# Performance work log

Measured on AMD Instinct MI355X. Metric: run time of the kernel, lower is better.

The kernel has to match this reference:

```python
import jax, jax.numpy as jnp
import numpy as np

B, N, D = 8, 2048, 512   # batch, ctx_size, input_size
P, H = 16, 32            # num_pers, hidden_size


def setup_inputs() -> dict:
    key = jax.random.key(0)
    k1, k2 = jax.random.split(key)
    context = jax.random.normal(k1, (B, N, D), dtype=jnp.float32)
    # stacked weights of the 16 bias-free nn.Linear(input_size, hidden_size) layers
    # xavier-uniform-style scale: sqrt(6/(fan_in+fan_out))
    limit = np.sqrt(6.0 / (D + H)).astype(np.float32)
    W = jax.random.uniform(k2, (P, H, D), dtype=jnp.float32, minval=-limit, maxval=limit)
    ctx_mask = jnp.ones((B, N), dtype=jnp.int32)
    return {"context": context, "W": W, "ctx_mask": ctx_mask}


def reference(context, W, ctx_mask):
    # per-persona projection + relu: [P, B, N, H]
    fc = jax.nn.relu(jnp.einsum('bnd,phd->pbnh', context, W))
    # sum over personas of fc @ fc^T, then average: [B, N, N]
    att = jnp.einsum('pbnh,pbmh->bnm', fc, fc) / P
    # NOTE: original uses F.softmax(attention, dim=1) -> softmax over rows (axis=1)
    att = jax.nn.softmax(att, axis=1)
    # masked_fill with markoff_value=0 on masked columns then masked rows
    m = ctx_mask.astype(att.dtype)          # [B, N]
    att = att * m[:, None, :] * m[:, :, None]
    return att
```

## Files before the change

### kernel.cpp

```cpp
#include <hip/hip_runtime.h>

#define Bc 8
#define Nc 2048
#define Dc 512
#define Pc 16
#define Hc 32
#define PH 512
#define M1 16384
#define NN 4194304

#define BM 128
#define BN 128
#define BK 32

typedef __attribute__((ext_vector_type(8))) short bf16x8;
typedef __attribute__((ext_vector_type(4))) float f32x4;

static __device__ __forceinline__ unsigned short f2b(float x) {
    union { float f; unsigned u; } v; v.f = x;
    unsigned r = v.u + 0x7fffu + ((v.u >> 16) & 1u);
    return (unsigned short)(r >> 16);
}

static __device__ __forceinline__ void load16_lds(const unsigned short* g, unsigned short* l) {
    __builtin_amdgcn_global_load_lds(
        (const __attribute__((address_space(1))) void*)g,
        (__attribute__((address_space(3))) void*)l,
        16, 0, 0);
}

__global__ __launch_bounds__(256) void prep_kernel(
    const float* __restrict__ ctx, const float* __restrict__ W,
    unsigned short* __restrict__ Xb, unsigned short* __restrict__ Wb,
    float* __restrict__ rsum) {
    int t = blockIdx.x * 256 + threadIdx.x;
    if (t < 2097152) {
        float4 v = ((const float4*)ctx)[t];
        ushort4 o;
        o.x = f2b(v.x); o.y = f2b(v.y); o.z = f2b(v.z); o.w = f2b(v.w);
        ((ushort4*)Xb)[t] = o;
    }
    if (t < 65536) {
        float4 v = ((const float4*)W)[t];
        ushort4 o;
        o.x = f2b(v.x); o.y = f2b(v.y); o.z = f2b(v.z); o.w = f2b(v.w);
        ((ushort4*)Wb)[t] = o;
    }
    if (t < 4096) {
        float4 z; z.x = 0.f; z.y = 0.f; z.z = 0.f; z.w = 0.f;
        ((float4*)rsum)[t] = z;
    }
}

__global__ __launch_bounds__(256) void gemm1_relu(
    const unsigned short* __restrict__ Xb, const unsigned short* __restrict__ Wb,
    unsigned short* __restrict__ F) {
    __shared__ unsigned short As[BM * BK];
    __shared__ unsigned short Bs[BN * BK];
    const int tid = threadIdx.x;
    const int lane = tid & 63;
    const int wave = tid >> 6;
    const int wm = wave >> 1, wn = wave & 1;
    const int row0 = blockIdx.y * BM;
    const int col0 = blockIdx.x * BN;

    f32x4 acc[4][4] = {};

    for (int k0 = 0; k0 < Dc; k0 += BK) {
#pragma unroll
        for (int j = 0; j < 2; ++j) {
            int e = j * 256 + tid;
            int rr = e >> 2, cc = e & 3;
            load16_lds(&Xb[(size_t)(row0 + rr) * Dc + k0 + cc * 8], &As[e * 8]);
            load16_lds(&Wb[(size_t)(col0 + rr) * Dc + k0 + cc * 8], &Bs[e * 8]);
        }
        __syncthreads();

        bf16x8 af[4], bfr[4];
#pragma unroll
        for (int i = 0; i < 4; ++i) {
            af[i]  = *(const bf16x8*)&As[(wm * 64 + i * 16 + (lane & 15)) * BK + (lane >> 4) * 8];
            bfr[i] = *(const bf16x8*)&Bs[(wn * 64 + i * 16 + (lane & 15)) * BK + (lane >> 4) * 8];
        }
#pragma unroll
        for (int mi = 0; mi < 4; ++mi)
#pragma unroll
            for (int ni = 0; ni < 4; ++ni)
                acc[mi][ni] = __builtin_amdgcn_mfma_f32_16x16x32_bf16(af[mi], bfr[ni], acc[mi][ni], 0, 0, 0);
        __syncthreads();
    }

#pragma unroll
    for (int mi = 0; mi < 4; ++mi) {
#pragma unroll
        for (int ni = 0; ni < 4; ++ni) {
            int col  = col0 + wn * 64 + ni * 16 + (lane & 15);
            int rowb = row0 + wm * 64 + mi * 16 + ((lane >> 4) << 2);
#pragma unroll
            for (int r = 0; r < 4; ++r) {
                float v = acc[mi][ni][r];
                v = fmaxf(v, 0.0f);
                F[(size_t)(rowb + r) * PH + col] = f2b(v);
            }
        }
    }
}

__global__ __launch_bounds__(256) void gemm2_exp(
    const unsigned short* __restrict__ F, float* __restrict__ out,
    float* __restrict__ rsum) {
    __shared__ unsigned short As[BM * BK];
    __shared__ unsigned short Bs[BN * BK];
    const int tid = threadIdx.x;
    const int lane = tid & 63;
    const int wave = tid >> 6;
    const int wm = wave >> 1, wn = wave & 1;
    const int b = blockIdx.z;
    const int row0 = blockIdx.y * BM;
    const int col0 = blockIdx.x * BN;
    const unsigned short* Fb = F + (size_t)b * Nc * PH;

    f32x4 acc[4][4] = {};

    for (int k0 = 0; k0 < PH; k0 += BK) {
#pragma unroll
        for (int j = 0; j < 2; ++j) {
            int e = j * 256 + tid;
            int rr = e >> 2, cc = e & 3;
            load16_lds(&Fb[(size_t)(row0 + rr) * PH + k0 + cc * 8], &As[e * 8]);
            load16_lds(&Fb[(size_t)(col0 + rr) * PH + k0 + cc * 8], &Bs[e * 8]);
        }
        __syncthreads();

        bf16x8 af[4], bfr[4];
#pragma unroll
        for (int i = 0; i < 4; ++i) {
            af[i]  = *(const bf16x8*)&As[(wm * 64 + i * 16 + (lane & 15)) * BK + (lane >> 4) * 8];
            bfr[i] = *(const bf16x8*)&Bs[(wn * 64 + i * 16 + (lane & 15)) * BK + (lane >> 4) * 8];
        }
#pragma unroll
        for (int mi = 0; mi < 4; ++mi)
#pragma unroll
            for (int ni = 0; ni < 4; ++ni)
                acc[mi][ni] = __builtin_amdgcn_mfma_f32_16x16x32_bf16(af[mi], bfr[ni], acc[mi][ni], 0, 0, 0);
        __syncthreads();
    }

    float csum[4] = {0.f, 0.f, 0.f, 0.f};
    float* outb = out + (size_t)b * NN;
#pragma unroll
    for (int mi = 0; mi < 4; ++mi) {
#pragma unroll
        for (int ni = 0; ni < 4; ++ni) {
            int col  = col0 + wn * 64 + ni * 16 + (lane & 15);
            int rowb = row0 + wm * 64 + mi * 16 + ((lane >> 4) << 2);
            float s4 = 0.f;
#pragma unroll
            for (int r = 0; r < 4; ++r) {
                float e = __expf(acc[mi][ni][r] * 0.0625f - 32.0f);
                outb[(size_t)(rowb + r) * Nc + col] = e;
                s4 += e;
            }
            csum[ni] += s4;
        }
    }
#pragma unroll
    for (int ni = 0; ni < 4; ++ni) {
        float s = csum[ni];
        s += __shfl_xor(s, 16);
        s += __shfl_xor(s, 32);
        if ((lane >> 4) == 0) {
            atomicAdd(&rsum[b * Nc + col0 + wn * 64 + ni * 16 + lane], s);
        }
    }
}

__global__ __launch_bounds__(256) void norm_kernel(
    float* __restrict__ out, const float* __restrict__ rsum,
    const int* __restrict__ mask) {
    int t = blockIdx.x * 256 + threadIdx.x;
    int idx4 = t << 2;
    int b  = idx4 >> 22;
    int n  = (idx4 >> 11) & 2047;
    int m0 = idx4 & 2047;
    float4 v = ((float4*)out)[t];
    const float4 rv = *(const float4*)&rsum[b * Nc + m0];
    float mr = (float)mask[b * Nc + n];
    int4 mc = *(const int4*)&mask[b * Nc + m0];
    v.x = v.x / rv.x * mr * (float)mc.x;
    v.y = v.y / rv.y * mr * (float)mc.y;
    v.z = v.z / rv.z * mr * (float)mc.z;
    v.w = v.w / rv.w * mr * (float)mc.w;
    ((float4*)out)[t] = v;
}

extern "C" void kernel_launch(void* const* d_in, const int* in_sizes, int n_in,
                              void* d_out, int out_size, void* d_ws, size_t ws_size,
                              hipStream_t stream) {
    const float* ctx  = (const float*)d_in[0];
    const float* W    = (const float*)d_in[1];
    const int*   mask = (const int*)d_in[2];
    float* out = (float*)d_out;

    char* ws = (char*)d_ws;
    unsigned short* Xb = (unsigned short*)ws;
    unsigned short* Wb = (unsigned short*)(ws + 16777216);
    unsigned short* F  = (unsigned short*)(ws + 16777216 + 524288);
    float* rsum        = (float*)(ws + 16777216 + 524288 + 16777216);

    prep_kernel<<<8192, 256, 0, stream>>>(ctx, W, Xb, Wb, rsum);
    gemm1_relu<<<dim3(4, 128), 256, 0, stream>>>(Xb, Wb, F);
    gemm2_exp<<<dim3(16, 16, 8), 256, 0, stream>>>(F, out, rsum);
    norm_kernel<<<32768, 256, 0, stream>>>(out, rsum, mask);
}
```

Before: 255.5 us.

## Recompute Gram tiles instead of storing and renormalizing unnormalized output

Replaces the store-exp-then-normalize scheme with two passes over the Gram matrix. The first pass computes only the column sums of exp, using the symmetry of F·F^T so that only the 136 upper-triangular tiles are processed, with each off-diagonal tile also contributing row sums. A small kernel then forms mask-scaled reciprocals. The second pass recomputes the full GEMM and writes the normalized, masked output once, which removes the 128 MB read-modify-write of the separate norm kernel at the cost of roughly 1.5x the GEMM2 compute.

```diff
diff --git a/kernel.cpp b/kernel.cpp
--- a/kernel.cpp
+++ b/kernel.cpp
@@ -3,10 +3,7 @@
 #define Bc 8
 #define Nc 2048
 #define Dc 512
-#define Pc 16
-#define Hc 32
 #define PH 512
-#define M1 16384
 #define NN 4194304
 
 #define BM 128
@@ -98,17 +95,111 @@
             int rowb = row0 + wm * 64 + mi * 16 + ((lane >> 4) << 2);
 #pragma unroll
             for (int r = 0; r < 4; ++r) {
-                float v = acc[mi][ni][r];
-                v = fmaxf(v, 0.0f);
+                float v = fmaxf(acc[mi][ni][r], 0.0f);
                 F[(size_t)(rowb + r) * PH + col] = f2b(v);
             }
         }
     }
 }
 
-__global__ __launch_bounds__(256) void gemm2_exp(
-    const unsigned short* __restrict__ F, float* __restrict__ out,
-    float* __restrict__ rsum) {
+__global__ __launch_bounds__(256) void gemm2_rsum(
+    const unsigned short* __restrict__ F, float* __restrict__ rsum) {
+    __shared__ unsigned short As[BM * BK];
+    __shared__ unsigned short Bs[BN * BK];
+    const int tid = threadIdx.x;
+    const int lane = tid & 63;
+    const int wave = tid >> 6;
+    const int wm = wave >> 1, wn = wave & 1;
+    const int b = blockIdx.y;
+
+    int idx = blockIdx.x;
+    int j = 0;
+    while (((j + 1) * (j + 2) / 2) <= idx) ++j;
+    int i = idx - j * (j + 1) / 2;
+    const int row0 = i * BM;
+    const int col0 = j * BN;
+    const unsigned short* Fb = F + (size_t)b * Nc * PH;
+
+    f32x4 acc[4][4] = {};
+
+    for (int k0 = 0; k0 < PH; k0 += BK) {
+#pragma unroll
+        for (int jj = 0; jj < 2; ++jj) {
+            int e = jj * 256 + tid;
+            int rr = e >> 2, cc = e & 3;
+            load16_lds(&Fb[(size_t)(row0 + rr) * PH + k0 + cc * 8], &As[e * 8]);
+            load16_lds(&Fb[(size_t)(col0 + rr) * PH + k0 + cc * 8], &Bs[e * 8]);
+        }
+        __syncthreads();
+
+        bf16x8 af[4], bfr[4];
+#pragma unroll
+        for (int q = 0; q < 4; ++q) {
+            af[q]  = *(const bf16x8*)&As[(wm * 64 + q * 16 + (lane & 15)) * BK + (lane >> 4) * 8];
+            bfr[q] = *(const bf16x8*)&Bs[(wn * 64 + q * 16 + (lane & 15)) * BK + (lane >> 4) * 8];
+        }
+#pragma unroll
+        for (int mi = 0; mi < 4; ++mi)
+#pragma unroll
+            for (int ni = 0; ni < 4; ++ni)
+                acc[mi][ni] = __builtin_amdgcn_mfma_f32_16x16x32_bf16(af[mi], bfr[ni], acc[mi][ni], 0, 0, 0);
+        __syncthreads();
+    }
+
+    float csum[4] = {0.f, 0.f, 0.f, 0.f};
+    float rsm[4][4];
+#pragma unroll
+    for (int mi = 0; mi < 4; ++mi)
+#pragma unroll
+        for (int r = 0; r < 4; ++r) rsm[mi][r] = 0.f;
+
+#pragma unroll
+    for (int mi = 0; mi < 4; ++mi) {
+#pragma unroll
+        for (int ni = 0; ni < 4; ++ni) {
+#pragma unroll
+            for (int r = 0; r < 4; ++r) {
+                float e = __expf(acc[mi][ni][r] * 0.0625f - 32.0f);
+                csum[ni] += e;
+                rsm[mi][r] += e;
+            }
+        }
+    }
+#pragma unroll
+    for (int ni = 0; ni < 4; ++ni) {
+        float s = csum[ni];
+        s += __shfl_xor(s, 16);
+        s += __shfl_xor(s, 32);
+        if ((lane >> 4) == 0)
+            atomicAdd(&rsum[b * Nc + col0 + wn * 64 + ni * 16 + lane], s);
+    }
+    if (i != j) {
+#pragma unroll
+        for (int mi = 0; mi < 4; ++mi) {
+#pragma unroll
+            for (int r = 0; r < 4; ++r) {
+                float s = rsm[mi][r];
+                s += __shfl_xor(s, 1);
+                s += __shfl_xor(s, 2);
+                s += __shfl_xor(s, 4);
+                s += __shfl_xor(s, 8);
+                if ((lane & 15) == 0)
+                    atomicAdd(&rsum[b * Nc + row0 + wm * 64 + mi * 16 + ((lane >> 4) << 2) + r], s);
+            }
+        }
+    }
+}
+
+__global__ __launch_bounds__(256) void invr_kernel(
+    const float* __restrict__ rsum, const int* __restrict__ mask,
+    float* __restrict__ invr) {
+    int t = blockIdx.x * 256 + threadIdx.x;
+    if (t < Bc * Nc) invr[t] = (float)mask[t] / rsum[t];
+}
+
+__global__ __launch_bounds__(256) void gemm2_write(
+    const unsigned short* __restrict__ F, const float* __restrict__ invr,
+    const int* __restrict__ mask, float* __restrict__ out) {
     __shared__ unsigned short As[BM * BK];
     __shared__ unsigned short Bs[BN * BK];
     const int tid = threadIdx.x;
@@ -124,8 +215,8 @@
 
     for (int k0 = 0; k0 < PH; k0 += BK) {
 #pragma unroll
-        for (int j = 0; j < 2; ++j) {
-            int e = j * 256 + tid;
+        for (int jj = 0; jj < 2; ++jj) {
+            int e = jj * 256 + tid;
             int rr = e >> 2, cc = e & 3;
             load16_lds(&Fb[(size_t)(row0 + rr) * PH + k0 + cc * 8], &As[e * 8]);
             load16_lds(&Fb[(size_t)(col0 + rr) * PH + k0 + cc * 8], &Bs[e * 8]);
@@ -134,9 +225,9 @@
 
         bf16x8 af[4], bfr[4];
 #pragma unroll
-        for (int i = 0; i < 4; ++i) {
-            af[i]  = *(const bf16x8*)&As[(wm * 64 + i * 16 + (lane & 15)) * BK + (lane >> 4) * 8];
-            bfr[i] = *(const bf16x8*)&Bs[(wn * 64 + i * 16 + (lane & 15)) * BK + (lane >> 4) * 8];
+        for (int q = 0; q < 4; ++q) {
+            af[q]  = *(const bf16x8*)&As[(wm * 64 + q * 16 + (lane & 15)) * BK + (lane >> 4) * 8];
+            bfr[q] = *(const bf16x8*)&Bs[(wn * 64 + q * 16 + (lane & 15)) * BK + (lane >> 4) * 8];
         }
 #pragma unroll
         for (int mi = 0; mi < 4; ++mi)
@@ -146,52 +237,27 @@
         __syncthreads();
     }
 
-    float csum[4] = {0.f, 0.f, 0.f, 0.f};
+    float iv[4];
+#pragma unroll
+    for (int ni = 0; ni < 4; ++ni)
+        iv[ni] = invr[b * Nc + col0 + wn * 64 + ni * 16 + (lane & 15)];
+
     float* outb = out + (size_t)b * NN;
 #pragma unroll
     for (int mi = 0; mi < 4; ++mi) {
+        int rowb = row0 + wm * 64 + mi * 16 + ((lane >> 4) << 2);
+        const int4 mr4 = *(const int4*)&mask[b * Nc + rowb];
+        float mr[4] = {(float)mr4.x, (float)mr4.y, (float)mr4.z, (float)mr4.w};
 #pragma unroll
         for (int ni = 0; ni < 4; ++ni) {
-            int col  = col0 + wn * 64 + ni * 16 + (lane & 15);
-            int rowb = row0 + wm * 64 + mi * 16 + ((lane >> 4) << 2);
-            float s4 = 0.f;
+            int col = col0 + wn * 64 + ni * 16 + (lane & 15);
 #pragma unroll
             for (int r = 0; r < 4; ++r) {
                 float e = __expf(acc[mi][ni][r] * 0.0625f - 32.0f);
-                outb[(size_t)(rowb + r) * Nc + col] = e;
-                s4 += e;
-            }
-            csum[ni] += s4;
-        }
-    }
-#pragma unroll
-    for (int ni = 0; ni < 4; ++ni) {
-        float s = csum[ni];
-        s += __shfl_xor(s, 16);
-        s += __shfl_xor(s, 32);
-        if ((lane >> 4) == 0) {
-            atomicAdd(&rsum[b * Nc + col0 + wn * 64 + ni * 16 + lane], s);
-        }
-    }
-}
-
-__global__ __launch_bounds__(256) void norm_kernel(
-    float* __restrict__ out, const float* __restrict__ rsum,
-    const int* __restrict__ mask) {
-    int t = blockIdx.x * 256 + threadIdx.x;
-    int idx4 = t << 2;
-    int b  = idx4 >> 22;
-    int n  = (idx4 >> 11) & 2047;
-    int m0 = idx4 & 2047;
-    float4 v = ((float4*)out)[t];
-    const float4 rv = *(const float4*)&rsum[b * Nc + m0];
-    float mr = (float)mask[b * Nc + n];
-    int4 mc = *(const int4*)&mask[b * Nc + m0];
-    v.x = v.x / rv.x * mr * (float)mc.x;
-    v.y = v.y / rv.y * mr * (float)mc.y;
-    v.z = v.z / rv.z * mr * (float)mc.z;
-    v.w = v.w / rv.w * mr * (float)mc.w;
-    ((float4*)out)[t] = v;
+                outb[(size_t)(rowb + r) * Nc + col] = e * iv[ni] * mr[r];
+            }
+        }
+    }
 }
 
 extern "C" void kernel_launch(void* const* d_in, const int* in_sizes, int n_in,
@@ -207,9 +273,11 @@
     unsigned short* Wb = (unsigned short*)(ws + 16777216);
     unsigned short* F  = (unsigned short*)(ws + 16777216 + 524288);
     float* rsum        = (float*)(ws + 16777216 + 524288 + 16777216);
+    float* invr        = (float*)(ws + 16777216 + 524288 + 16777216 + 65536);
 
     prep_kernel<<<8192, 256, 0, stream>>>(ctx, W, Xb, Wb, rsum);
     gemm1_relu<<<dim3(4, 128), 256, 0, stream>>>(Xb, Wb, F);
-    gemm2_exp<<<dim3(16, 16, 8), 256, 0, stream>>>(F, out, rsum);
-    norm_kernel<<<32768, 256, 0, stream>>>(out, rsum, mask);
-}
+    gemm2_rsum<<<dim3(136, 8), 256, 0, stream>>>(F, rsum);
+    invr_kernel<<<64, 256, 0, stream>>>(rsum, mask, invr);
+    gemm2_write<<<dim3(16, 16, 8), 256, 0, stream>>>(F, invr, mask, out);
+}
```

Result: no change. 253.1 us (-0.9%).
